# Optimization experiments

Measured on AMD Instinct MI355X. Metric: run time of the kernel, lower is better.

The kernel has to match this reference:

```python
import jax, jax.numpy as jnp
import numpy as np

B, S, D, H, DH, F, K = 16, 1024, 384, 2, 192, 1536, 9  # batch, seq, d_model, heads, d_head, filter, kernel
EPS = 1e-5


def setup_inputs() -> dict:
    key = jax.random.key(0)
    ks = jax.random.split(key, 20)
    p = lambda k, shape: jax.random.normal(k, shape, dtype=jnp.float32) * 0.02
    return {
        "x": jax.random.normal(ks[0], (B, S, D), dtype=jnp.float32),
        "mask": jax.random.randint(ks[1], (B, S, S), 0, 2).astype(bool),
        # per-head QKV projections stacked over heads: [H, D, DH], biases [H, DH]
        "Wq": p(ks[2], (H, D, DH)), "bq": p(ks[3], (H, DH)),
        "Wk": p(ks[4], (H, D, DH)), "bk": p(ks[5], (H, DH)),
        "Wv": p(ks[6], (H, D, DH)), "bv": p(ks[7], (H, DH)),
        "Wo": p(ks[8], (D, D)), "bo": p(ks[9], (D,)),
        # conv kernels in lax WIO layout: [K, in, out] (== torch [out,in,K] transposed)
        "Wc1": p(ks[10], (K, D, F)), "bc1": p(ks[11], (F,)),
        "Wc2": p(ks[12], (K, F, D)), "bc2": p(ks[13], (D,)),
        "g1": jnp.ones((D,), jnp.float32), "beta1": jnp.zeros((D,), jnp.float32),
        "g2": jnp.ones((D,), jnp.float32), "beta2": jnp.zeros((D,), jnp.float32),
    }


def _layernorm(x, g, b):
    m = jnp.mean(x, axis=-1, keepdims=True)
    v = jnp.var(x, axis=-1, keepdims=True)
    return (x - m) / jnp.sqrt(v + EPS) * g + b


def reference(x, mask, Wq, bq, Wk, bk, Wv, bv, Wo, bo, Wc1, bc1, Wc2, bc2, g1, beta1, g2, beta2):
    residual = x
    # multi-head attention (heads vectorized instead of python loop)
    Q = jnp.einsum('bsd,hde->bhse', x, Wq) + bq[None, :, None, :]
    Kt = jnp.einsum('bsd,hde->bhse', x, Wk) + bk[None, :, None, :]
    V = jnp.einsum('bsd,hde->bhse', x, Wv) + bv[None, :, None, :]
    # NOTE: original scales by sqrt(d_model), not sqrt(d_head) — kept faithful
    QK = jnp.einsum('bhse,bhte->bhst', Q, Kt) / np.sqrt(D).astype(np.float32)
    QK = jnp.where(mask[:, None, :, :], jnp.float32(-1e9), QK)  # QK[mask] = -1e9
    A = jax.nn.softmax(QK, axis=-1)
    O = jnp.einsum('bhst,bhte->bhse', A, V)
    O = O.transpose(0, 2, 1, 3).reshape(O.shape[0], O.shape[2], H * DH)  # concat heads
    attn = O @ Wo + bo
    x = _layernorm(attn + residual, g1, beta1)  # dropout=0 (eval) is identity
    residual = x
    # conv1d FFN, padding='same'
    h = jax.lax.conv_general_dilated(x, Wc1, (1,), 'SAME', dimension_numbers=('NWC', 'WIO', 'NWC')) + bc1
    h = jax.nn.relu(h)
    h = jax.lax.conv_general_dilated(h, Wc2, (1,), 'SAME', dimension_numbers=('NWC', 'WIO', 'NWC')) + bc2
    x = _layernorm(h + residual, g2, beta2)
    return x
```

## Files before the change

### kernel.cpp

```cpp
#include <hip/hip_runtime.h>
#include <hip/hip_bf16.h>
#include <stdint.h>
#include <math.h>

typedef __attribute__((ext_vector_type(8))) short bf16x8;
typedef __attribute__((ext_vector_type(4))) float f32x4;
typedef __attribute__((ext_vector_type(4))) unsigned short u16x4;

#define DEV static __device__ __forceinline__

DEV unsigned short f2bf(float f){
  union { float f; unsigned u; } v; v.f = f;
  unsigned r = v.u + 0x7fffu + ((v.u >> 16) & 1u);
  return (unsigned short)(r >> 16);
}

DEV void gload_lds16(const void* g, void* l){
  __builtin_amdgcn_global_load_lds(
      (const __attribute__((address_space(1))) unsigned int*)g,
      (__attribute__((address_space(3))) unsigned int*)l, 16, 0, 0);
}


__global__ __launch_bounds__(256) void k_misc(const unsigned char* __restrict__ mb,
                                              unsigned* __restrict__ flag,
                                              unsigned short* __restrict__ zp){
  __shared__ unsigned s;
  if(threadIdx.x==0) s = 0;
  __syncthreads();
  unsigned any = 0;
  for(int off = threadIdx.x; off < 4096; off += 256) if(off & 3) any |= mb[off];
  if(any) atomicOr(&s, 1u);
  __syncthreads();
  if(threadIdx.x==0) *flag = (s ? 1u : 0u);
  for(int i = threadIdx.x; i < 2048; i += 256) zp[i] = 0;
}

__global__ __launch_bounds__(256) void k_cast4(const float* __restrict__ x,
                                               unsigned short* __restrict__ o, int n4){
  for(int i = blockIdx.x*256 + threadIdx.x; i < n4; i += gridDim.x*256){
    f32x4 v = ((const f32x4*)x)[i];
    u16x4 r;
    #pragma unroll
    for(int j=0;j<4;++j) r[j] = f2bf(v[j]);
    ((u16x4*)o)[i] = r;
  }
}

__global__ __launch_bounds__(256) void k_prep_qkv(const float* __restrict__ Wq, const float* __restrict__ Wk,
                                                  const float* __restrict__ Wv, const float* __restrict__ bq,
                                                  const float* __restrict__ bk, const float* __restrict__ bv,
                                                  unsigned short* __restrict__ Wt, float* __restrict__ bias){
  const int total = 1152*384;
  for(int idx = blockIdx.x*blockDim.x + threadIdx.x; idx < total; idx += gridDim.x*blockDim.x){
    int n = idx/384, d = idx%384;
    int mat = n/384, rem = n%384, h = rem/192, e = rem%192;
    const float* W = (mat==0) ? Wq : ((mat==1) ? Wk : Wv);
    Wt[idx] = f2bf(W[((size_t)h*384 + d)*192 + e]);
    if(d==0){
      const float* bb = (mat==0) ? bq : ((mat==1) ? bk : bv);
      bias[n] = bb[h*192 + e];
    }
  }
}

__global__ __launch_bounds__(256) void k_tr(const float* __restrict__ src,
                                            unsigned short* __restrict__ dst, int R, int C){
  __shared__ float t[32][33];
  const int tx = threadIdx.x & 31, ty = threadIdx.x >> 5;
  const int c0 = blockIdx.x*32, r0 = blockIdx.y*32;
  #pragma unroll
  for(int i=0;i<32;i+=8) t[ty+i][tx] = src[(size_t)(r0+ty+i)*C + c0+tx];
  __syncthreads();
  #pragma unroll
  for(int i=0;i<32;i+=8) dst[(size_t)(c0+ty+i)*R + r0+tx] = f2bf(t[tx][ty+i]);
}


template<int CIN, int NOUT>
__global__ __launch_bounds__(256)
void k_prepB(const float* __restrict__ W, unsigned short* __restrict__ Bf){
  constexpr int DTOT = CIN/64;
  const int gid = blockIdx.x*256 + threadIdx.x;
  const int lane = gid & 63;
  const int frag = gid >> 6;
  int f = frag;
  const int kk2 = f & 1, fn = (f>>1) & 3; f >>= 3;
  const int d = f % DTOT; f /= DTOT;
  const int t = f % 9;
  const int nq = f / 9;
  const int lane16 = lane & 15, laneh = lane >> 4;
  const int n = nq*64 + fn*16 + lane16;
  const int kbase = t*CIN + d*64 + kk2*32 + laneh*8;
  bf16x8 out;
  #pragma unroll
  for(int j=0;j<8;++j)
    out[j] = (short)f2bf(W[(size_t)(kbase + j)*NOUT + n]);
  *(bf16x8*)(Bf + (size_t)frag*512 + lane*8) = out;
}


template<int EPI>
__global__ __launch_bounds__(256)
void k_gemm(const unsigned short* __restrict__ A,
            const unsigned short* __restrict__ Bt,
            const float* __restrict__ bias,
            unsigned short* __restrict__ out_q,
            unsigned short* __restrict__ out_k,
            unsigned short* __restrict__ out_v,
            float* __restrict__ out_f,
            int Ktot, int lda)
{
  constexpr int BK = 64;
  __shared__ __attribute__((aligned(16))) unsigned short As[128*64];
  __shared__ __attribute__((aligned(16))) unsigned short Bs[128*64];
  const int tid = threadIdx.x;
  const int wave = tid >> 6, lane = tid & 63;
  const int lane16 = lane & 15, laneh = lane >> 4;
  const int wm = wave >> 1, wn = wave & 1;

  const int nwg  = gridDim.x*gridDim.y;
  const int flat = blockIdx.y*gridDim.x + blockIdx.x;
  const int swz  = (flat & 7)*(nwg >> 3) + (flat >> 3);
  const int m0 = (swz % gridDim.y) * 128;
  const int n0 = (swz / gridDim.y) * 128;

  f32x4 acc[4][4];
  #pragma unroll
  for(int i=0;i<4;++i)
    #pragma unroll
    for(int j=0;j<4;++j) acc[i][j] = (f32x4){0.f,0.f,0.f,0.f};

  const int nsteps = Ktot / BK;
  for(int ks=0; ks<nsteps; ++ks){
    const int kg = ks*BK;
    __syncthreads();
    #pragma unroll
    for(int q=0;q<4;++q){
      int e0 = (q*256 + tid)*8;
      int row = e0 >> 6, col = e0 & 63;
      gload_lds16(A + (size_t)(m0+row)*lda + kg + col, (char*)As + q*4096 + wave*1024);
    }
    #pragma unroll
    for(int q=0;q<4;++q){
      int e0 = (q*256 + tid)*8;
      int row = e0 >> 6, col = e0 & 63;
      gload_lds16(Bt + (size_t)(n0+row)*Ktot + kg + col, (char*)Bs + q*4096 + wave*1024);
    }
    __syncthreads();
    #pragma unroll
    for(int kk=0; kk<BK; kk+=32){
      bf16x8 af[4], bfr[4];
      #pragma unroll
      for(int fm=0;fm<4;++fm)
        af[fm] = *(const bf16x8*)&As[(wm*64 + fm*16 + lane16)*64 + kk + laneh*8];
      #pragma unroll
      for(int fn=0;fn<4;++fn)
        bfr[fn] = *(const bf16x8*)&Bs[(wn*64 + fn*16 + lane16)*64 + kk + laneh*8];
      #pragma unroll
      for(int fm=0;fm<4;++fm)
        #pragma unroll
        for(int fn=0;fn<4;++fn)
          acc[fm][fn] = __builtin_amdgcn_mfma_f32_16x16x32_bf16(af[fm], bfr[fn], acc[fm][fn], 0, 0, 0);
    }
  }
  #pragma unroll
  for(int fm=0;fm<4;++fm){
    #pragma unroll
    for(int fn=0;fn<4;++fn){
      #pragma unroll
      for(int r=0;r<4;++r){
        int gr = m0 + wm*64 + fm*16 + laneh*4 + r;
        int gc = n0 + wn*64 + fn*16 + lane16;
        float c = acc[fm][fn][r] + bias[gc];
        if(EPI==0){
          int mat = gc/384, rem = gc%384, h = rem/192, e = rem%192;
          int b = gr >> 10, s = gr & 1023;
          int bh = b*2 + h;
          if(mat==0)      out_q[((size_t)bh*1024 + s)*192 + e] = f2bf(c);
          else if(mat==1) out_k[((size_t)bh*1024 + s)*192 + e] = f2bf(c);
          else            out_v[((size_t)bh*192 + e)*1024 + s] = f2bf(c);
        } else {
          out_f[(size_t)gr*384 + gc] = c;
        }
      }
    }
  }
}


template<int EPI, int CIN, int NOUT>
__global__ __launch_bounds__(256)
void k_conv(const unsigned short* __restrict__ A,
            const unsigned short* __restrict__ Bf,
            const float* __restrict__ bias,
            unsigned short* __restrict__ out_h,
            float* __restrict__ out_f,
            float* __restrict__ out_f2,
            const unsigned short* __restrict__ zp)
{
  __shared__ __attribute__((aligned(16))) unsigned short Ah[160*64];
  const int tid = threadIdx.x;
  const int wave = tid >> 6, lane = tid & 63;
  const int lane16 = lane & 15, laneh = lane >> 4;
  const int wm = wave >> 1, wn = wave & 1;

  const int nwg  = gridDim.x*gridDim.y;
  const int flat = blockIdx.y*gridDim.x + blockIdx.x;
  const int swz  = (flat & 7)*(nwg >> 3) + (flat >> 3);
  const int m0 = (swz % gridDim.y) * 128;
  const int n0 = (swz / gridDim.y) * 128;

  constexpr int DTOT = CIN/64;
  const int dper = DTOT / gridDim.z;
  const int dlo  = blockIdx.z * dper;
  const int srow = m0 & 1023;
  const int nq   = (n0 >> 6) + wn;

  f32x4 acc[4][4];
  #pragma unroll
  for(int i=0;i<4;++i)
    #pragma unroll
    for(int j=0;j<4;++j) acc[i][j] = (f32x4){0.f,0.f,0.f,0.f};

  for(int db=0; db<dper; ++db){
    const int dblk = dlo + db;
    if(db) __syncthreads();
    #pragma unroll
    for(int q=0;q<5;++q){
      int P = (q*256 + tid)*16;
      int row = P >> 7, cb = P & 127;
      int cs  = (cb ^ ((row&7)<<4)) >> 1;
      int s = srow - 4 + row;
      const unsigned short* src = (s >= 0 && s < 1024)
          ? A + (size_t)(m0 - 4 + row)*CIN + dblk*64 + cs : zp;
      gload_lds16(src, (char*)Ah + q*4096 + wave*1024);
    }
    __syncthreads();
    #pragma unroll
    for(int t=0; t<9; ++t){
      const unsigned short* fb = Bf + ((size_t)((nq*9 + t)*DTOT) + dblk)*4096 + lane*8;
      bf16x8 bfr[2][4];
      #pragma unroll
      for(int fn=0; fn<4; ++fn){
        bfr[0][fn] = *(const bf16x8*)(fb + (fn*2+0)*512);
        bfr[1][fn] = *(const bf16x8*)(fb + (fn*2+1)*512);
      }
      #pragma unroll
      for(int kk2=0; kk2<2; ++kk2){
        #pragma unroll
        for(int fm=0; fm<4; ++fm){
          int ra = wm*64 + fm*16 + lane16 + t;
          bf16x8 af = *(const bf16x8*)((const char*)Ah +
              ra*128 + (((kk2*32 + laneh*8)*2) ^ ((ra&7)<<4)));
          #pragma unroll
          for(int fn=0; fn<4; ++fn)
            acc[fm][fn] = __builtin_amdgcn_mfma_f32_16x16x32_bf16(af, bfr[kk2][fn], acc[fm][fn], 0, 0, 0);
        }
      }
    }
  }
  float* out_p = (EPI==3 && blockIdx.z==2) ? out_f2
               : out_f + (size_t)blockIdx.z * 16384 * 384;
  #pragma unroll
  for(int fm=0;fm<4;++fm){
    #pragma unroll
    for(int fn=0;fn<4;++fn){
      #pragma unroll
      for(int r=0;r<4;++r){
        int gr = m0 + wm*64 + fm*16 + laneh*4 + r;
        int gc = n0 + wn*64 + fn*16 + lane16;
        float c = acc[fm][fn][r];
        if(EPI==2){
          c += bias[gc];
          out_h[(size_t)gr*NOUT + gc] = f2bf(fmaxf(c, 0.f));
        } else {
          out_p[(size_t)gr*384 + gc] = c;
        }
      }
    }
  }
}

__global__ __launch_bounds__(256)
void k_bias(const float* __restrict__ p, const float* __restrict__ bias,
            float* __restrict__ out, int n4){
  for(int i = blockIdx.x*256 + threadIdx.x; i < n4; i += gridDim.x*256){
    f32x4 a = ((const f32x4*)p)[i];
    f32x4 bi = ((const f32x4*)bias)[i % 96];
    ((f32x4*)out)[i] = a + bi;
  }
}


__global__ __launch_bounds__(256)
void k_attn(const unsigned short* __restrict__ Q,
            const unsigned short* __restrict__ Kb,
            const unsigned short* __restrict__ Vt,
            const void* __restrict__ mask,
            const unsigned* __restrict__ flag,
            unsigned short* __restrict__ O)
{
  __shared__ __attribute__((aligned(16))) unsigned short Ks[64*192];
  __shared__ __attribute__((aligned(16))) unsigned short Vs[192*64];
  __shared__ __attribute__((aligned(16))) unsigned short P_lds[4*16*64];

  const int flat = blockIdx.y*gridDim.x + blockIdx.x;
  const int w = (flat & 7)*64 + (flat >> 3);
  const int bh = w >> 4, qb = w & 15;
  const int b = bh >> 1, h = bh & 1;
  const int tid = threadIdx.x;
  const int wave = tid >> 6, lane = tid & 63;
  const int lane16 = lane & 15, laneh = lane >> 4;
  const int q0 = qb*64 + wave*16;
  const bool mbyte = (*flag != 0);
  const unsigned char* m8 = (const unsigned char*)mask;
  const int* m32 = (const int*)mask;
  unsigned short* Pw = P_lds + wave*1024;

  bf16x8 qa[6];
  {
    const unsigned short* Qrow = Q + ((size_t)bh*1024 + q0 + lane16)*192 + laneh*8;
    #pragma unroll
    for(int kk=0; kk<6; ++kk) qa[kk] = *(const bf16x8*)(Qrow + kk*32);
  }

  f32x4 accO[12];
  #pragma unroll
  for(int i=0;i<12;++i) accO[i] = (f32x4){0.f,0.f,0.f,0.f};
  float mrow[4], lrow[4];
  #pragma unroll
  for(int r=0;r<4;++r){ mrow[r] = -1e30f; lrow[r] = 0.f; }

  const float rs = 0.05103103630798288f;
  const size_t mbase = (size_t)b * 1024 * 1024;
  const unsigned short* Kbh = Kb + (size_t)bh*1024*192;
  const unsigned short* Vbh = Vt + (size_t)bh*192*1024;

  for(int t0=0; t0<1024; t0+=64){
    unsigned mskv[4][4];
    #pragma unroll
    for(int tf=0; tf<4; ++tf){
      #pragma unroll
      for(int r=0;r<4;++r){
        size_t mi = mbase + (size_t)(q0 + laneh*4 + r)*1024 + t0 + tf*16 + lane16;
        mskv[tf][r] = mbyte ? (unsigned)m8[mi] : (unsigned)m32[mi];
      }
    }
    __syncthreads();
    #pragma unroll
    for(int q=0;q<6;++q){
      int P = (q*256 + tid)*16;
      int row = P/384, cb = P%384;
      gload_lds16(Kbh + (size_t)(t0 + row)*192 + ((cb ^ ((row&7)<<4)) >> 1),
                  (char*)Ks + q*4096 + wave*1024);
    }
    #pragma unroll
    for(int q=0;q<6;++q){
      int P = (q*256 + tid)*16;
      int row = P >> 7, cb = P & 127;
      gload_lds16(Vbh + (size_t)row*1024 + t0 + ((cb ^ ((row&7)<<4)) >> 1),
                  (char*)Vs + q*4096 + wave*1024);
    }
    __syncthreads();
    f32x4 sc[4];
    #pragma unroll
    for(int i=0;i<4;++i) sc[i] = (f32x4){0.f,0.f,0.f,0.f};
    #pragma unroll
    for(int kk=0; kk<6; ++kk){
      #pragma unroll
      for(int tf=0; tf<4; ++tf){
        int tt = tf*16 + lane16;
        const bf16x8* kp = (const bf16x8*)((const char*)Ks +
            tt*384 + ((kk*64 + laneh*16) ^ ((tt&7)<<4)));
        sc[tf] = __builtin_amdgcn_mfma_f32_16x16x32_bf16(qa[kk], *kp, sc[tf], 0, 0, 0);
      }
    }
    #pragma unroll
    for(int tf=0; tf<4; ++tf)
      #pragma unroll
      for(int r=0;r<4;++r)
        sc[tf][r] = mskv[tf][r] ? -1e9f : sc[tf][r]*rs;
    float tm[4];
    #pragma unroll
    for(int r=0;r<4;++r){
      float v = fmaxf(fmaxf(sc[0][r],sc[1][r]), fmaxf(sc[2][r],sc[3][r]));
      v = fmaxf(v, __shfl_xor(v,1)); v = fmaxf(v, __shfl_xor(v,2));
      v = fmaxf(v, __shfl_xor(v,4)); v = fmaxf(v, __shfl_xor(v,8));
      tm[r] = v;
    }
    float scale_o[4];
    #pragma unroll
    for(int r=0;r<4;++r){
      float mn = fmaxf(mrow[r], tm[r]);
      scale_o[r] = __expf(mrow[r] - mn);
      mrow[r] = mn;
    }
    float ts[4] = {0.f,0.f,0.f,0.f};
    #pragma unroll
    for(int tf=0; tf<4; ++tf){
      #pragma unroll
      for(int r=0;r<4;++r){
        float p = __expf(sc[tf][r] - mrow[r]);
        ts[r] += p;
        Pw[(laneh*4 + r)*64 + tf*16 + lane16] = f2bf(p);
      }
    }
    #pragma unroll
    for(int r=0;r<4;++r){
      float v = ts[r];
      v += __shfl_xor(v,1); v += __shfl_xor(v,2); v += __shfl_xor(v,4); v += __shfl_xor(v,8);
      lrow[r] = lrow[r]*scale_o[r] + v;
    }
    #pragma unroll
    for(int ef=0; ef<12; ++ef)
      #pragma unroll
      for(int r=0;r<4;++r) accO[ef][r] *= scale_o[r];
    #pragma unroll
    for(int kk=0; kk<64; kk+=32){
      bf16x8 pa = *(const bf16x8*)&Pw[lane16*64 + kk + laneh*8];
      #pragma unroll
      for(int ef=0; ef<12; ++ef){
        int er = ef*16 + lane16;
        const bf16x8* vp = (const bf16x8*)((const char*)Vs +
            er*128 + (((kk + laneh*8)*2) ^ ((er&7)<<4)));
        accO[ef] = __builtin_amdgcn_mfma_f32_16x16x32_bf16(pa, *vp, accO[ef], 0, 0, 0);
      }
    }
  }
  #pragma unroll
  for(int ef=0; ef<12; ++ef){
    #pragma unroll
    for(int r=0;r<4;++r){
      int qr = q0 + laneh*4 + r;
      int e  = ef*16 + lane16;
      float o = accO[ef][r] / lrow[r];
      O[((size_t)b*1024 + qr)*384 + h*192 + e] = f2bf(o);
    }
  }
}


__global__ __launch_bounds__(256)
void k_ln(const float* __restrict__ a, const float* __restrict__ resid,
          const float* __restrict__ g, const float* __restrict__ beta,
          float* __restrict__ outf, unsigned short* __restrict__ outbf)
{
  const int row = blockIdx.x*4 + (threadIdx.x >> 6);
  const int lane = threadIdx.x & 63;
  const float* pa = a + (size_t)row*384;
  const float* pr = resid + (size_t)row*384;
  float v[6], s = 0.f, s2 = 0.f;
  #pragma unroll
  for(int j=0;j<6;++j){
    int e = lane + j*64;
    float t = pa[e] + pr[e];
    v[j] = t; s += t; s2 += t*t;
  }
  #pragma unroll
  for(int o=1;o<64;o<<=1){ s += __shfl_xor(s,o); s2 += __shfl_xor(s2,o); }
  float mean = s * (1.f/384.f);
  float var  = s2 * (1.f/384.f) - mean*mean;
  float inv  = rsqrtf(var + 1e-5f);
  #pragma unroll
  for(int j=0;j<6;++j){
    int e = lane + j*64;
    float t = (v[j]-mean)*inv*g[e] + beta[e];
    if(outf)  outf[(size_t)row*384 + e] = t;
    if(outbf) outbf[(size_t)row*384 + e] = f2bf(t);
  }
}

__global__ __launch_bounds__(256)
void k_lnred3(const float* __restrict__ p0, const float* __restrict__ p2,
              const float* __restrict__ bias, const float* __restrict__ resid,
              const float* __restrict__ g, const float* __restrict__ beta,
              float* __restrict__ outf)
{
  const int row = blockIdx.x*4 + (threadIdx.x >> 6);
  const int lane = threadIdx.x & 63;
  const float* p1 = p0 + (size_t)16384*384;
  const size_t base = (size_t)row*384;
  float v[6], s = 0.f, s2 = 0.f;
  #pragma unroll
  for(int j=0;j<6;++j){
    int e = lane + j*64;
    float t = p0[base+e] + p1[base+e] + p2[base+e] + bias[e] + resid[base+e];
    v[j] = t; s += t; s2 += t*t;
  }
  #pragma unroll
  for(int o=1;o<64;o<<=1){ s += __shfl_xor(s,o); s2 += __shfl_xor(s2,o); }
  float mean = s * (1.f/384.f);
  float var  = s2 * (1.f/384.f) - mean*mean;
  float inv  = rsqrtf(var + 1e-5f);
  #pragma unroll
  for(int j=0;j<6;++j){
    int e = lane + j*64;
    outf[base + e] = (v[j]-mean)*inv*g[e] + beta[e];
  }
}


extern "C" void kernel_launch(void* const* d_in, const int* in_sizes, int n_in,
                              void* d_out, int out_size, void* d_ws, size_t ws_size,
                              hipStream_t stream)
{
  const float* x   = (const float*)d_in[0];
  const void*  mask= d_in[1];
  const float* Wq  = (const float*)d_in[2];
  const float* bq  = (const float*)d_in[3];
  const float* Wk  = (const float*)d_in[4];
  const float* bk  = (const float*)d_in[5];
  const float* Wv  = (const float*)d_in[6];
  const float* bv  = (const float*)d_in[7];
  const float* Wo  = (const float*)d_in[8];
  const float* bo  = (const float*)d_in[9];
  const float* Wc1 = (const float*)d_in[10];
  const float* bc1 = (const float*)d_in[11];
  const float* Wc2 = (const float*)d_in[12];
  const float* bc2 = (const float*)d_in[13];
  const float* g1  = (const float*)d_in[14];
  const float* be1 = (const float*)d_in[15];
  const float* g2  = (const float*)d_in[16];
  const float* be2 = (const float*)d_in[17];

  char* ws = (char*)d_ws;
  size_t off = 0;
  auto alloc = [&](size_t bytes)->char*{
    char* p = ws + off; off += (bytes + 255) & ~(size_t)255; return p;
  };
  unsigned short* zp   = (unsigned short*)alloc(4096);
  unsigned*       flag = (unsigned*)alloc(256);
  unsigned short* wqkv = (unsigned short*)alloc((size_t)1152*384*2);
  float*          bqkv = (float*)alloc((size_t)1152*4);
  unsigned short* wot  = (unsigned short*)alloc((size_t)384*384*2);
  unsigned short* wc1t = (unsigned short*)alloc((size_t)1536*3456*2);
  unsigned short* wc2t = (unsigned short*)alloc((size_t)384*13824*2);
  unsigned short* xbf  = (unsigned short*)alloc((size_t)16384*384*2);
  unsigned short* Qb   = (unsigned short*)alloc((size_t)32*1024*192*2);
  unsigned short* Kbuf = (unsigned short*)alloc((size_t)32*1024*192*2);
  unsigned short* Vt   = (unsigned short*)alloc((size_t)32*192*1024*2);
  float*          yb   = (float*)alloc((size_t)16384*384*4);
  unsigned short* hb   = (unsigned short*)alloc((size_t)16384*1536*2);
  unsigned short* Obf  = xbf;
  unsigned short* x1bf = Qb;
  float*          x1f  = (float*)Kbuf;
  float*          zb   = yb;
  const size_t pb_bytes = (size_t)2*16384*384*4;
  const bool   splitk   = (ws_size >= off + pb_bytes);
  float*       pb       = (float*)alloc(pb_bytes);
  float*       slab2    = (float*)xbf;

  k_misc<<<1,256,0,stream>>>((const unsigned char*)mask, flag, zp);
  k_cast4<<<2048,256,0,stream>>>(x, xbf, 16384*384/4);
  k_prep_qkv<<<1728,256,0,stream>>>(Wq,Wk,Wv,bq,bk,bv,wqkv,bqkv);
  k_tr<<<dim3(12,12),256,0,stream>>>(Wo, wot, 384, 384);
  k_prepB<384,1536><<<2592,256,0,stream>>>(Wc1, wc1t);
  k_prepB<1536,384><<<2592,256,0,stream>>>(Wc2, wc2t);

  k_gemm<0><<<dim3(9,128),256,0,stream>>>(xbf, wqkv, bqkv, Qb, Kbuf, Vt,
                                          nullptr, 384, 384);
  k_attn<<<dim3(16,32),256,0,stream>>>(Qb, Kbuf, Vt, mask, flag, Obf);
  k_gemm<1><<<dim3(3,128),256,0,stream>>>(Obf, wot, bo, nullptr,nullptr,nullptr,
                                          yb, 384, 384);
  k_ln<<<4096,256,0,stream>>>(yb, x, g1, be1, x1f, x1bf);
  k_conv<2,384,1536><<<dim3(12,128,1),256,0,stream>>>(x1bf, wc1t, bc1, hb, nullptr, nullptr, zp);
  if(splitk){
    k_conv<3,1536,384><<<dim3(3,128,3),256,0,stream>>>(hb, wc2t, nullptr, nullptr, pb, slab2, zp);
    k_lnred3<<<4096,256,0,stream>>>(pb, slab2, bc2, x1f, g2, be2, (float*)d_out);
  } else {
    k_conv<3,1536,384><<<dim3(3,128,1),256,0,stream>>>(hb, wc2t, nullptr, nullptr, zb, nullptr, zp);
    k_bias<<<2048,256,0,stream>>>(zb, bc2, zb, 16384*384/4);
    k_ln<<<4096,256,0,stream>>>(zb, x1f, g2, be2, (float*)d_out, nullptr);
  }
}
```

Before: 543.9 us.

## Widen conv tile N dimension to reuse staged A rows across more output columns

The conv kernels are templated on FN, the number of 16-wide N fragments per wave, and conv1 now uses 128x256 tiles while conv2 uses 128x384 tiles covering the full output width. Each LDS-staged activation block is then reused across more output columns, so the same A rows are reloaded by fewer workgroups. B fragments are loaded per kk2 step instead of all up front, and launch bounds ask for 2 workgroups per SIMD. The larger accumulator arrays (up to 48 f32x4 per thread) raise register pressure and may cause spills. Conv2 now launches only 128 or 384 workgroups, which risks underfilling the GPU.

Measured after the change: 1.544 ms. +183.9%, slower.

```diff
diff --git a/kernel.cpp b/kernel.cpp
--- a/kernel.cpp
+++ b/kernel.cpp
@@ -189,8 +189,8 @@
 }
 
 
-template<int EPI, int CIN, int NOUT>
-__global__ __launch_bounds__(256)
+template<int EPI, int CIN, int NOUT, int FN>
+__global__ __launch_bounds__(256, 2)
 void k_conv(const unsigned short* __restrict__ A,
             const unsigned short* __restrict__ Bf,
             const float* __restrict__ bias,
@@ -209,19 +209,19 @@
   const int flat = blockIdx.y*gridDim.x + blockIdx.x;
   const int swz  = (flat & 7)*(nwg >> 3) + (flat >> 3);
   const int m0 = (swz % gridDim.y) * 128;
-  const int n0 = (swz / gridDim.y) * 128;
+  const int n0 = (swz / gridDim.y) * (FN*32);
 
   constexpr int DTOT = CIN/64;
   const int dper = DTOT / gridDim.z;
   const int dlo  = blockIdx.z * dper;
   const int srow = m0 & 1023;
-  const int nq   = (n0 >> 6) + wn;
-
-  f32x4 acc[4][4];
+  const int nqb  = (n0 >> 6) + wn*(FN/4);
+
+  f32x4 acc[4][FN];
   #pragma unroll
   for(int i=0;i<4;++i)
     #pragma unroll
-    for(int j=0;j<4;++j) acc[i][j] = (f32x4){0.f,0.f,0.f,0.f};
+    for(int j=0;j<FN;++j) acc[i][j] = (f32x4){0.f,0.f,0.f,0.f};
 
   for(int db=0; db<dper; ++db){
     const int dblk = dlo + db;
@@ -239,23 +239,23 @@
     __syncthreads();
     #pragma unroll
     for(int t=0; t<9; ++t){
-      const unsigned short* fb = Bf + ((size_t)((nq*9 + t)*DTOT) + dblk)*4096 + lane*8;
-      bf16x8 bfr[2][4];
-      #pragma unroll
-      for(int fn=0; fn<4; ++fn){
-        bfr[0][fn] = *(const bf16x8*)(fb + (fn*2+0)*512);
-        bfr[1][fn] = *(const bf16x8*)(fb + (fn*2+1)*512);
-      }
       #pragma unroll
       for(int kk2=0; kk2<2; ++kk2){
+        bf16x8 af[4];
         #pragma unroll
         for(int fm=0; fm<4; ++fm){
           int ra = wm*64 + fm*16 + lane16 + t;
-          bf16x8 af = *(const bf16x8*)((const char*)Ah +
+          af[fm] = *(const bf16x8*)((const char*)Ah +
               ra*128 + (((kk2*32 + laneh*8)*2) ^ ((ra&7)<<4)));
+        }
+        #pragma unroll
+        for(int fn=0; fn<FN; ++fn){
+          const int nq = nqb + (fn>>2);
+          bf16x8 bfr = *(const bf16x8*)(Bf +
+              ((size_t)(((nq*9 + t)*DTOT + dblk)*8) + (fn&3)*2 + kk2)*512 + lane*8);
           #pragma unroll
-          for(int fn=0; fn<4; ++fn)
-            acc[fm][fn] = __builtin_amdgcn_mfma_f32_16x16x32_bf16(af, bfr[kk2][fn], acc[fm][fn], 0, 0, 0);
+          for(int fm=0; fm<4; ++fm)
+            acc[fm][fn] = __builtin_amdgcn_mfma_f32_16x16x32_bf16(af[fm], bfr, acc[fm][fn], 0, 0, 0);
         }
       }
     }
@@ -265,11 +265,11 @@
   #pragma unroll
   for(int fm=0;fm<4;++fm){
     #pragma unroll
-    for(int fn=0;fn<4;++fn){
+    for(int fn=0;fn<FN;++fn){
       #pragma unroll
       for(int r=0;r<4;++r){
         int gr = m0 + wm*64 + fm*16 + laneh*4 + r;
-        int gc = n0 + wn*64 + fn*16 + lane16;
+        int gc = n0 + wn*(FN*16) + (fn>>2)*64 + (fn&3)*16 + lane16;
         float c = acc[fm][fn][r];
         if(EPI==2){
           c += bias[gc];
@@ -564,12 +564,12 @@
   k_gemm<1><<<dim3(3,128),256,0,stream>>>(Obf, wot, bo, nullptr,nullptr,nullptr,
                                           yb, 384, 384);
   k_ln<<<4096,256,0,stream>>>(yb, x, g1, be1, x1f, x1bf);
-  k_conv<2,384,1536><<<dim3(12,128,1),256,0,stream>>>(x1bf, wc1t, bc1, hb, nullptr, nullptr, zp);
+  k_conv<2,384,1536,8><<<dim3(6,128,1),256,0,stream>>>(x1bf, wc1t, bc1, hb, nullptr, nullptr, zp);
   if(splitk){
-    k_conv<3,1536,384><<<dim3(3,128,3),256,0,stream>>>(hb, wc2t, nullptr, nullptr, pb, slab2, zp);
+    k_conv<3,1536,384,12><<<dim3(1,128,3),256,0,stream>>>(hb, wc2t, nullptr, nullptr, pb, slab2, zp);
     k_lnred3<<<4096,256,0,stream>>>(pb, slab2, bc2, x1f, g2, be2, (float*)d_out);
   } else {
-    k_conv<3,1536,384><<<dim3(3,128,1),256,0,stream>>>(hb, wc2t, nullptr, nullptr, zb, nullptr, zp);
+    k_conv<3,1536,384,12><<<dim3(1,128,1),256,0,stream>>>(hb, wc2t, nullptr, nullptr, zb, nullptr, zp);
     k_bias<<<2048,256,0,stream>>>(zb, bc2, zb, 16384*384/4);
     k_ln<<<4096,256,0,stream>>>(zb, x1f, g2, be2, (float*)d_out, nullptr);
   }
```
